# Performance work log

Hardware: AMD Instinct MI355X
Metric: run time of the kernel (lower is better)

Reference implementation:

```python
import jax, jax.numpy as jnp
import numpy as np
from jax import lax

RATES = (2, 3, 5, 9)
C_IN = 64
B, H, W = 4, 128, 128


def conv2d(x, w, b, dilation):
    # x: [B,C,H,W], w: [O,I,3,3]; padding=dilation keeps spatial size
    y = lax.conv_general_dilated(
        x, w, window_strides=(1, 1),
        padding=[(dilation, dilation), (dilation, dilation)],
        rhs_dilation=(dilation, dilation),
        dimension_numbers=('NCHW', 'OIHW', 'NCHW'))
    return y + b[None, :, None, None]


def bilinear_sample(x, py, px):
    # x: [B,C,H,W]; py,px: [B,K,H,W] float sampling positions; zeros outside
    Hh, Ww = x.shape[-2], x.shape[-1]
    y0 = jnp.floor(py)
    x0 = jnp.floor(px)
    wy1 = py - y0
    wx1 = px - x0
    wy0 = 1.0 - wy1
    wx0 = 1.0 - wx1

    def gather(yi, xi):
        valid = (yi >= 0) & (yi < Hh) & (xi >= 0) & (xi < Ww)
        yc = jnp.clip(yi, 0, Hh - 1).astype(jnp.int32)
        xc = jnp.clip(xi, 0, Ww - 1).astype(jnp.int32)
        # per-batch fancy gather: [C,K,H,W]
        vals = jax.vmap(lambda im, yy, xx: im[:, yy, xx])(x, yc, xc)
        return vals * valid[:, None].astype(x.dtype)

    out = (gather(y0, x0) * (wy0 * wx0)[:, None]
           + gather(y0, x0 + 1) * (wy0 * wx1)[:, None]
           + gather(y0 + 1, x0) * (wy1 * wx0)[:, None]
           + gather(y0 + 1, x0 + 1) * (wy1 * wx1)[:, None])
    return out  # [B,C,K,H,W]


def deform_conv(x, offset, weight, dilation):
    # offset: [B,18,H,W] = (dy,dx) per kernel point; weight: [O,C,3,3]
    b, c, h, w = x.shape
    K = 9
    off = offset.reshape(b, K, 2, h, w)
    dy, dx = off[:, :, 0], off[:, :, 1]
    ky = jnp.repeat((jnp.arange(3) - 1) * dilation, 3).astype(x.dtype)  # [9]
    kx = jnp.tile((jnp.arange(3) - 1) * dilation, 3).astype(x.dtype)
    hh = jnp.arange(h, dtype=x.dtype)[None, None, :, None]
    ww = jnp.arange(w, dtype=x.dtype)[None, None, None, :]
    py = hh + ky[None, :, None, None] + dy
    px = ww + kx[None, :, None, None] + dx
    sampled = bilinear_sample(x, py, px)  # [B,C,K,H,W]
    w9 = weight.reshape(weight.shape[0], c, K)
    return jnp.einsum('bckhw,ock->bohw', sampled, w9)


def setup_inputs() -> dict:
    key = jax.random.key(0)
    ks = jax.random.split(key, 8)
    s = 0.05
    return {
        'x': jax.random.normal(ks[0], (B, C_IN, H, W), jnp.float32),
        'dw': jax.random.normal(ks[1], (4, C_IN, C_IN, 3, 3), jnp.float32) * s,
        'ow': jax.random.normal(ks[2], (4, 18, C_IN, 3, 3), jnp.float32) * s,
        'ob': jax.random.normal(ks[3], (4, 18), jnp.float32) * s,
        'se_w1': jax.random.normal(ks[4], (C_IN, 4 * C_IN), jnp.float32) * s,
        'se_b1': jax.random.normal(ks[5], (C_IN,), jnp.float32) * s,
        'se_w2': jax.random.normal(ks[6], (4 * C_IN, C_IN), jnp.float32) * s,
        'se_b2': jax.random.normal(ks[7], (4 * C_IN,), jnp.float32) * s,
    }


def reference(x, dw, ow, ob, se_w1, se_b1, se_w2, se_b2):
    b, c, h, w = x.shape
    outs = []
    for i in range(4):
        j = (i - 1) % 4  # faithful to `self.offsets[i - 1]` in the source
        off = jax.nn.relu(conv2d(x, ow[j], ob[j], RATES[j]))
        outs.append(deform_conv(x, off, dw[i], RATES[i]))
    cat = jnp.concatenate(outs, axis=1)  # [B,4C,H,W]
    # SENet on concatenated features
    g = cat.mean(axis=(2, 3))  # [B,4C]
    h1 = jax.nn.relu(g @ se_w1.T + se_b1)
    s = jax.nn.sigmoid(h1 @ se_w2.T + se_b2)  # [B,4C]
    gated = (1.0 + s)[:, :, None, None] * cat
    fused = gated.reshape(b, 4, c, h, w).sum(axis=1)  # sum over the 4 stages
    return x + fused
```

## Files before the change

kernel.cpp:

```cpp
#include <hip/hip_runtime.h>
#include <hip/hip_bf16.h>
#include <math.h>

#define BATCH 4
#define CIN 64
#define HH 128
#define WW 128
#define HWP (HH*WW)

#define OFF_OFF   0
#define CAT_OFF   4718592
#define XHWC_OFF  (CAT_OFF + 8388608)
#define WTH_OFF   (XHWC_OFF + 2097152)
#define OWH_OFF   (WTH_OFF + 73728)
#define G_OFF     (OWH_OFF + 36864)
#define SCALE_OFF (G_OFF + 1024)

typedef _Float16 h16x2 __attribute__((ext_vector_type(2)));
typedef _Float16 h16x8 __attribute__((ext_vector_type(8)));
typedef float    f32x4 __attribute__((ext_vector_type(4)));

union h8view { h16x8 v8; h16x2 v2[4]; };

__device__ __forceinline__ int rate_of(int i) {
    return (i == 0) ? 2 : (i == 1) ? 3 : (i == 2) ? 5 : 9;
}

__global__ __launch_bounds__(256) void prep_kernel(
    const float* __restrict__ dw, const float* __restrict__ ow,
    _Float16* __restrict__ wth, _Float16* __restrict__ owh)
{
    int idx = blockIdx.x * 256 + threadIdx.x;
    if (idx < 147456) {
        int c = idx & 63;
        int k = (idx >> 6) % 9;
        int r = idx / 576;
        int o = r & 63;
        int i = r >> 6;
        wth[idx] = (_Float16)dw[((i * 64 + o) * 64 + c) * 9 + k];
        return;
    }
    int idx2 = idx - 147456;
    if (idx2 < 73728) {
        int c = idx2 & 63;
        int r = idx2 >> 6;
        int o = r & 31;
        int r2 = r >> 5;
        int tap = r2 % 9;
        int j = r2 / 9;
        owh[idx2] = (o < 18) ? (_Float16)ow[((j * 18 + o) * 64 + c) * 9 + tap]
                             : (_Float16)0.f;
    }
}

__global__ __launch_bounds__(256) void xhwc_kernel(
    const float* __restrict__ x, _Float16* __restrict__ xhwc)
{
    const int t  = threadIdx.x;
    const int b  = blockIdx.y;
    const int p0 = blockIdx.x * 64;
    const int px = t & 63;
    const int cO = t >> 6;

    const float* xb = x + (size_t)b * CIN * HWP + p0 + px;
    _Float16* xh = xhwc + ((size_t)b * HWP + p0 + px) * 64;

#pragma unroll
    for (int g = 0; g < 2; ++g) {
        const int cb = cO * 8 + g * 32;
        h16x8 v;
#pragma unroll
        for (int cj = 0; cj < 8; ++cj)
            v[cj] = (_Float16)xb[(size_t)(cb + cj) * HWP];
        *(h16x8*)(xh + cb) = v;
    }
}

__global__ __launch_bounds__(256) void offset_mfma_kernel(
    const _Float16* __restrict__ xhwc, const _Float16* __restrict__ owh,
    const float* __restrict__ ob, float* __restrict__ off)
{
    __shared__ __align__(16) _Float16 S2[2][64][72];

    const int t  = threadIdx.x;
    const int z  = blockIdx.y;
    const int j  = z >> 2, b = z & 3;
    const int d  = rate_of(j);
    const int p0 = blockIdx.x * 64;
    const int ph = p0 >> 7;
    const int cb0 = p0 & 127;

    const int wv = t >> 6, lane = t & 63;
    const int nl = lane & 15, quad = lane >> 4;

    const _Float16* xh = xhwc + (size_t)b * HWP * 64;

    f32x4 acc[2];
    acc[0] = (f32x4){0.f, 0.f, 0.f, 0.f};
    acc[1] = (f32x4){0.f, 0.f, 0.f, 0.f};

    h16x8 v[2];

    auto stage_load = [&](int kk) {
        const int iy = kk / 3, ix = kk % 3;
        const int ys = ph + (iy - 1) * d;
        const bool rowok = (unsigned)ys < (unsigned)HH;
#pragma unroll
        for (int q = 0; q < 2; ++q) {
            const int task = q * 256 + t;
            const int px = task >> 3, ch = task & 7;
            const int xs = cb0 + px + (ix - 1) * d;
            h16x8 vv = {};
            if (rowok && (unsigned)xs < (unsigned)WW)
                vv = *(const h16x8*)(xh + ((size_t)(ys * WW + xs)) * 64 + ch * 8);
            v[q] = vv;
        }
    };
    auto stage_store = [&](int buf) {
#pragma unroll
        for (int q = 0; q < 2; ++q) {
            const int task = q * 256 + t;
            const int px = task >> 3, ch = task & 7;
            *(h16x8*)&S2[buf][px][ch * 8] = v[q];
        }
    };

    stage_load(0);
    stage_store(0);
    __syncthreads();

    for (int k = 0; k < 9; ++k) {
        if (k < 8) stage_load(k + 1);

#pragma unroll
        for (int q2 = 0; q2 < 2; ++q2) {
            h16x8 a = *(const h16x8*)&S2[k & 1][wv * 16 + nl][q2 * 32 + quad * 8];
#pragma unroll
            for (int nt = 0; nt < 2; ++nt) {
                const _Float16* brow = owh
                    + ((size_t)((j * 9 + k) * 32 + nt * 16 + nl)) * 64;
                h16x8 bf = *(const h16x8*)&brow[q2 * 32 + quad * 8];
                acc[nt] = __builtin_amdgcn_mfma_f32_16x16x32_f16(a, bf, acc[nt], 0, 0, 0);
            }
        }

        if (k < 8) stage_store((k + 1) & 1);
        __syncthreads();
    }

    float* op = off + (size_t)z * 18 * HWP + p0;
#pragma unroll
    for (int nt = 0; nt < 2; ++nt) {
        const int o = nt * 16 + nl;
        if (o < 18) {
            const float bias = ob[j * 18 + o];
#pragma unroll
            for (int r = 0; r < 4; ++r) {
                const int pxl = wv * 16 + quad * 4 + r;
                op[(size_t)o * HWP + pxl] = fmaxf(acc[nt][r] + bias, 0.f);
            }
        }
    }
}

__global__ __launch_bounds__(256) void deform_mfma_kernel(
    const _Float16* __restrict__ xhwc, const _Float16* __restrict__ wth,
    const float* __restrict__ off, _Float16* __restrict__ cat)
{
    __shared__ __align__(16) _Float16 S[2][128][72];

    const int t  = threadIdx.x;
    const int z  = blockIdx.y;
    const int i  = z >> 2, b = z & 3;
    const int d  = rate_of(i);
    const int j  = (i + 3) & 3;
    const int ty = blockIdx.x >> 1;
    const int tx = blockIdx.x & 1;

    const int chunk = t & 7;
    const int pxb   = t >> 3;
    const int cb    = chunk * 8;

    const int wv = t >> 6, lane = t & 63;
    const int nl = lane & 15, quad = lane >> 4;

    const _Float16* xh = xhwc + (size_t)b * HWP * 64;
    const float* offb = off + ((size_t)(j * 4 + b) * 18) * HWP;

    int phv[4], pwv[4], pgv[4];
#pragma unroll
    for (int it = 0; it < 4; ++it) {
        const int psub = it * 32 + pxb;
        phv[it] = ty * 2 + (psub >> 6);
        pwv[it] = tx * 64 + (psub & 63);
        pgv[it] = phv[it] * WW + pwv[it];
    }

    f32x4 acc[8];
#pragma unroll
    for (int a = 0; a < 8; ++a) acc[a] = (f32x4){0.f, 0.f, 0.f, 0.f};

    h8view u[4][4];
    h16x2  wp[4][4];
    float  ocy[4], ocx[4];
    float  ony[4], onx[4];

    auto gather = [&](int kk) {
        const int iy = kk / 3, ix = kk % 3;
#pragma unroll
        for (int it = 0; it < 4; ++it) {
            float py = (float)(phv[it] + (iy - 1) * d) + ocy[it];
            float px = (float)(pwv[it] + (ix - 1) * d) + ocx[it];
            float fy0 = floorf(py), fx0 = floorf(px);
            float wy1 = py - fy0, wx1 = px - fx0;
            float wy0 = 1.f - wy1, wx0 = 1.f - wx1;
            int y0 = (int)fy0, x0 = (int)fx0;
            int y1 = y0 + 1,  x1 = x0 + 1;
            bool vy0 = (unsigned)y0 < (unsigned)HH, vy1 = (unsigned)y1 < (unsigned)HH;
            bool vx0 = (unsigned)x0 < (unsigned)WW, vx1 = (unsigned)x1 < (unsigned)WW;
            int yc0 = min(max(y0, 0), HH - 1), yc1 = min(max(y1, 0), HH - 1);
            int xc0 = min(max(x0, 0), WW - 1), xc1 = min(max(x1, 0), WW - 1);
            float w00 = (vy0 && vx0) ? wy0 * wx0 : 0.f;
            float w01 = (vy0 && vx1) ? wy0 * wx1 : 0.f;
            float w10 = (vy1 && vx0) ? wy1 * wx0 : 0.f;
            float w11 = (vy1 && vx1) ? wy1 * wx1 : 0.f;
            const _Float16 h00 = (_Float16)w00, h01 = (_Float16)w01;
            const _Float16 h10 = (_Float16)w10, h11 = (_Float16)w11;
            wp[it][0] = (h16x2){h00, h00};
            wp[it][1] = (h16x2){h01, h01};
            wp[it][2] = (h16x2){h10, h10};
            wp[it][3] = (h16x2){h11, h11};
            u[it][0].v8 = *(const h16x8*)(xh + (size_t)(yc0 * WW + xc0) * 64 + cb);
            u[it][1].v8 = *(const h16x8*)(xh + (size_t)(yc0 * WW + xc1) * 64 + cb);
            u[it][2].v8 = *(const h16x8*)(xh + (size_t)(yc1 * WW + xc0) * 64 + cb);
            u[it][3].v8 = *(const h16x8*)(xh + (size_t)(yc1 * WW + xc1) * 64 + cb);
        }
    };

    auto blendstore = [&](int buf) {
#pragma unroll
        for (int it = 0; it < 4; ++it) {
            h8view outv;
#pragma unroll
            for (int pp = 0; pp < 4; ++pp)
                outv.v2[pp] = u[it][0].v2[pp] * wp[it][0] + u[it][1].v2[pp] * wp[it][1]
                            + u[it][2].v2[pp] * wp[it][2] + u[it][3].v2[pp] * wp[it][3];
            *(h16x8*)&S[buf][it * 32 + pxb][cb] = outv.v8;
        }
    };

#pragma unroll
    for (int it = 0; it < 4; ++it) {
        ocy[it] = offb[0 * HWP + pgv[it]];
        ocx[it] = offb[1 * HWP + pgv[it]];
    }
    gather(0);
    blendstore(0);
#pragma unroll
    for (int it = 0; it < 4; ++it) {
        ocy[it] = offb[2 * HWP + pgv[it]];
        ocx[it] = offb[3 * HWP + pgv[it]];
    }
    __syncthreads();

    for (int k = 0; k < 9; ++k) {
        if (k < 8) {
            gather(k + 1);
            if (k < 7) {
#pragma unroll
                for (int it = 0; it < 4; ++it) {
                    ony[it] = offb[(2 * (k + 2)) * HWP + pgv[it]];
                    onx[it] = offb[(2 * (k + 2) + 1) * HWP + pgv[it]];
                }
            }
        }

#pragma unroll
        for (int q2 = 0; q2 < 2; ++q2) {
            h16x8 b0 = *(const h16x8*)&S[k & 1][wv * 32 + nl][q2 * 32 + quad * 8];
            h16x8 b1 = *(const h16x8*)&S[k & 1][wv * 32 + 16 + nl][q2 * 32 + quad * 8];
#pragma unroll
            for (int mt = 0; mt < 4; ++mt) {
                const _Float16* wrow = wth
                    + ((size_t)((i * 64 + mt * 16 + nl) * 9 + k)) * 64;
                h16x8 a = *(const h16x8*)&wrow[q2 * 32 + quad * 8];
                acc[mt * 2 + 0] = __builtin_amdgcn_mfma_f32_16x16x32_f16(a, b0, acc[mt * 2 + 0], 0, 0, 0);
                acc[mt * 2 + 1] = __builtin_amdgcn_mfma_f32_16x16x32_f16(a, b1, acc[mt * 2 + 1], 0, 0, 0);
            }
        }

        if (k < 8) {
            blendstore((k + 1) & 1);
#pragma unroll
            for (int it = 0; it < 4; ++it) { ocy[it] = ony[it]; ocx[it] = onx[it]; }
        }
        __syncthreads();
    }

#pragma unroll
    for (int mt = 0; mt < 4; ++mt) {
#pragma unroll
        for (int nt = 0; nt < 2; ++nt) {
            const int psub = wv * 32 + nt * 16 + nl;
            const int prow = ty * 2 + (psub >> 6);
            const int pcol = tx * 64 + (psub & 63);
            _Float16* cp = cat
                + ((size_t)(b * 256 + i * 64 + mt * 16 + quad * 4)) * HWP
                + prow * WW + pcol;
            const f32x4 v = acc[mt * 2 + nt];
#pragma unroll
            for (int r = 0; r < 4; ++r)
                cp[(size_t)r * HWP] = (_Float16)v[r];
        }
    }
}

__global__ __launch_bounds__(256) void reduce_kernel(
    const _Float16* __restrict__ cat, float* __restrict__ g)
{
    const int bc = blockIdx.x;
    const _Float16* p = cat + (size_t)bc * HWP;
    float s = 0.f;
#pragma unroll
    for (int q = 0; q < 8; ++q) {
        h16x8 v8 = *(const h16x8*)(p + q * 2048 + threadIdx.x * 8);
#pragma unroll
        for (int e = 0; e < 8; ++e) s += (float)v8[e];
    }
#pragma unroll
    for (int o = 32; o > 0; o >>= 1) s += __shfl_down(s, o, 64);
    __shared__ float ls[4];
    if ((threadIdx.x & 63) == 0) ls[threadIdx.x >> 6] = s;
    __syncthreads();
    if (threadIdx.x == 0) {
        g[bc] = (ls[0] + ls[1] + ls[2] + ls[3]) * (1.f / (float)HWP);
    }
}

__global__ __launch_bounds__(256) void se_kernel(
    const float* __restrict__ g,  const float* __restrict__ w1,
    const float* __restrict__ b1, const float* __restrict__ w2,
    const float* __restrict__ b2, float* __restrict__ scale)
{
    __shared__ float gs[1024];
    __shared__ float h1s[256];
    const int t = threadIdx.x;
#pragma unroll
    for (int q = 0; q < 4; ++q) gs[q * 256 + t] = g[q * 256 + t];
    __syncthreads();
    {
        int b = t >> 6, o = t & 63;
        float a = b1[o];
        for (int c = 0; c < 256; ++c)
            a = fmaf(gs[b * 256 + c], w1[o * 256 + c], a);
        h1s[t] = fmaxf(a, 0.f);
    }
    __syncthreads();
#pragma unroll
    for (int q = 0; q < 4; ++q) {
        int idx = q * 256 + t;
        int b = idx >> 8, cc = idx & 255;
        float a = b2[cc];
#pragma unroll 8
        for (int o = 0; o < 64; ++o)
            a = fmaf(h1s[b * 64 + o], w2[cc * 64 + o], a);
        scale[idx] = 1.f + 1.f / (1.f + expf(-a));
    }
}

__global__ __launch_bounds__(256) void final_kernel(
    const float* __restrict__ x, const _Float16* __restrict__ cat,
    const float* __restrict__ scale, float* __restrict__ out)
{
    const int gid = blockIdx.x;
    const int p = (gid & 63) * 256 + threadIdx.x;
    const int c = (gid >> 6) & 63;
    const int b = gid >> 12;
    const float s0 = scale[b * 256 + c];
    const float s1 = scale[b * 256 + 64 + c];
    const float s2 = scale[b * 256 + 128 + c];
    const float s3 = scale[b * 256 + 192 + c];
    const _Float16* cb = cat + ((size_t)(b * 256 + c)) * HWP + p;
    float v = x[(size_t)(b * 64 + c) * HWP + p];
    v = fmaf(s0, (float)cb[0 * 64 * HWP], v);
    v = fmaf(s1, (float)cb[1 * 64 * HWP], v);
    v = fmaf(s2, (float)cb[2 * 64 * HWP], v);
    v = fmaf(s3, (float)cb[3 * 64 * HWP], v);
    out[(size_t)(b * 64 + c) * HWP + p] = v;
}

extern "C" void kernel_launch(void* const* d_in, const int* in_sizes, int n_in,
                              void* d_out, int out_size, void* d_ws, size_t ws_size,
                              hipStream_t stream) {
    const float* x  = (const float*)d_in[0];
    const float* dw = (const float*)d_in[1];
    const float* ow = (const float*)d_in[2];
    const float* ob = (const float*)d_in[3];
    const float* w1 = (const float*)d_in[4];
    const float* b1 = (const float*)d_in[5];
    const float* w2 = (const float*)d_in[6];
    const float* b2 = (const float*)d_in[7];
    float* out = (float*)d_out;
    float* ws  = (float*)d_ws;

    float* OFF      = ws + OFF_OFF;
    _Float16* CAT   = (_Float16*)(ws + CAT_OFF);
    _Float16* XHWC  = (_Float16*)(ws + XHWC_OFF);
    _Float16* WTH   = (_Float16*)(ws + WTH_OFF);
    _Float16* OWH   = (_Float16*)(ws + OWH_OFF);
    float* G        = ws + G_OFF;
    float* SCALE    = ws + SCALE_OFF;

    prep_kernel<<<864, 256, 0, stream>>>(dw, ow, WTH, OWH);
    xhwc_kernel<<<dim3(256, 4), 256, 0, stream>>>(x, XHWC);
    offset_mfma_kernel<<<dim3(256, 16), 256, 0, stream>>>(XHWC, OWH, ob, OFF);
    deform_mfma_kernel<<<dim3(128, 16), 256, 0, stream>>>(XHWC, WTH, OFF, CAT);
    reduce_kernel<<<1024, 256, 0, stream>>>(CAT, G);
    se_kernel<<<1, 256, 0, stream>>>(G, w1, b1, w2, b2, SCALE);
    final_kernel<<<16384, 256, 0, stream>>>(x, CAT, SCALE, out);
}
```

Baseline: 305.4 us.

## Reuse staged halo row across kx taps in offset conv; single-buffer LDS

The offset convolution now stages one input row with a 2*d halo per kernel row (3 stages instead of 9), so the three horizontal taps read shifted windows from the same LDS tile instead of reloading from global memory. Both the offset and deform kernels drop from double-buffered to single-buffered shared memory and add an extra barrier before each store. This cuts global loads and LDS footprint, which may raise occupancy, at the cost of more synchronisation and less overlap between loads and MFMA work.

```diff
diff --git a/kernel.cpp b/kernel.cpp
--- a/kernel.cpp
+++ b/kernel.cpp
@@ -80,7 +80,7 @@
     const _Float16* __restrict__ xhwc, const _Float16* __restrict__ owh,
     const float* __restrict__ ob, float* __restrict__ off)
 {
-    __shared__ __align__(16) _Float16 S2[2][64][72];
+    __shared__ __align__(16) _Float16 S2[82][72];
 
     const int t  = threadIdx.x;
     const int z  = blockIdx.y;
@@ -95,56 +95,67 @@
 
     const _Float16* xh = xhwc + (size_t)b * HWP * 64;
 
+    const int width = 64 + 2 * d;
+    const int ntask = width * 8;
+
     f32x4 acc[2];
     acc[0] = (f32x4){0.f, 0.f, 0.f, 0.f};
     acc[1] = (f32x4){0.f, 0.f, 0.f, 0.f};
 
-    h16x8 v[2];
-
-    auto stage_load = [&](int kk) {
-        const int iy = kk / 3, ix = kk % 3;
-        const int ys = ph + (iy - 1) * d;
+    h16x8 sv[3];
+
+    auto stage_load = [&](int g) {
+        const int ys = ph + (g - 1) * d;
         const bool rowok = (unsigned)ys < (unsigned)HH;
 #pragma unroll
-        for (int q = 0; q < 2; ++q) {
+        for (int q = 0; q < 3; ++q) {
             const int task = q * 256 + t;
-            const int px = task >> 3, ch = task & 7;
-            const int xs = cb0 + px + (ix - 1) * d;
             h16x8 vv = {};
-            if (rowok && (unsigned)xs < (unsigned)WW)
-                vv = *(const h16x8*)(xh + ((size_t)(ys * WW + xs)) * 64 + ch * 8);
-            v[q] = vv;
+            if (task < ntask) {
+                const int sp = task >> 3, ch = task & 7;
+                const int xs = cb0 - d + sp;
+                if (rowok && (unsigned)xs < (unsigned)WW)
+                    vv = *(const h16x8*)(xh + ((size_t)(ys * WW + xs)) * 64 + ch * 8);
+            }
+            sv[q] = vv;
         }
     };
-    auto stage_store = [&](int buf) {
-#pragma unroll
-        for (int q = 0; q < 2; ++q) {
+    auto stage_store = [&]() {
+#pragma unroll
+        for (int q = 0; q < 3; ++q) {
             const int task = q * 256 + t;
-            const int px = task >> 3, ch = task & 7;
-            *(h16x8*)&S2[buf][px][ch * 8] = v[q];
+            if (task < ntask) {
+                const int sp = task >> 3, ch = task & 7;
+                *(h16x8*)&S2[sp][ch * 8] = sv[q];
+            }
         }
     };
 
     stage_load(0);
-    stage_store(0);
+    stage_store();
     __syncthreads();
 
-    for (int k = 0; k < 9; ++k) {
-        if (k < 8) stage_load(k + 1);
-
-#pragma unroll
-        for (int q2 = 0; q2 < 2; ++q2) {
-            h16x8 a = *(const h16x8*)&S2[k & 1][wv * 16 + nl][q2 * 32 + quad * 8];
-#pragma unroll
-            for (int nt = 0; nt < 2; ++nt) {
-                const _Float16* brow = owh
-                    + ((size_t)((j * 9 + k) * 32 + nt * 16 + nl)) * 64;
-                h16x8 bf = *(const h16x8*)&brow[q2 * 32 + quad * 8];
-                acc[nt] = __builtin_amdgcn_mfma_f32_16x16x32_f16(a, bf, acc[nt], 0, 0, 0);
-            }
-        }
-
-        if (k < 8) stage_store((k + 1) & 1);
+    for (int g = 0; g < 3; ++g) {
+        if (g < 2) stage_load(g + 1);
+
+#pragma unroll
+        for (int ix = 0; ix < 3; ++ix) {
+            const int k = g * 3 + ix;
+#pragma unroll
+            for (int q2 = 0; q2 < 2; ++q2) {
+                h16x8 a = *(const h16x8*)&S2[wv * 16 + nl + ix * d][q2 * 32 + quad * 8];
+#pragma unroll
+                for (int nt = 0; nt < 2; ++nt) {
+                    const _Float16* brow = owh
+                        + ((size_t)((j * 9 + k) * 32 + nt * 16 + nl)) * 64;
+                    h16x8 bf = *(const h16x8*)&brow[q2 * 32 + quad * 8];
+                    acc[nt] = __builtin_amdgcn_mfma_f32_16x16x32_f16(a, bf, acc[nt], 0, 0, 0);
+                }
+            }
+        }
+
+        __syncthreads();
+        if (g < 2) stage_store();
         __syncthreads();
     }
 
@@ -167,7 +178,7 @@
     const _Float16* __restrict__ xhwc, const _Float16* __restrict__ wth,
     const float* __restrict__ off, _Float16* __restrict__ cat)
 {
-    __shared__ __align__(16) _Float16 S[2][128][72];
+    __shared__ __align__(16) _Float16 S[128][72];
 
     const int t  = threadIdx.x;
     const int z  = blockIdx.y;
@@ -237,7 +248,7 @@
         }
     };
 
-    auto blendstore = [&](int buf) {
+    auto blendstore = [&]() {
 #pragma unroll
         for (int it = 0; it < 4; ++it) {
             h8view outv;
@@ -245,7 +256,7 @@
             for (int pp = 0; pp < 4; ++pp)
                 outv.v2[pp] = u[it][0].v2[pp] * wp[it][0] + u[it][1].v2[pp] * wp[it][1]
                             + u[it][2].v2[pp] * wp[it][2] + u[it][3].v2[pp] * wp[it][3];
-            *(h16x8*)&S[buf][it * 32 + pxb][cb] = outv.v8;
+            *(h16x8*)&S[it * 32 + pxb][cb] = outv.v8;
         }
     };
 
@@ -255,7 +266,7 @@
         ocx[it] = offb[1 * HWP + pgv[it]];
     }
     gather(0);
-    blendstore(0);
+    blendstore();
 #pragma unroll
     for (int it = 0; it < 4; ++it) {
         ocy[it] = offb[2 * HWP + pgv[it]];
@@ -277,8 +288,8 @@
 
 #pragma unroll
         for (int q2 = 0; q2 < 2; ++q2) {
-            h16x8 b0 = *(const h16x8*)&S[k & 1][wv * 32 + nl][q2 * 32 + quad * 8];
-            h16x8 b1 = *(const h16x8*)&S[k & 1][wv * 32 + 16 + nl][q2 * 32 + quad * 8];
+            h16x8 b0 = *(const h16x8*)&S[wv * 32 + nl][q2 * 32 + quad * 8];
+            h16x8 b1 = *(const h16x8*)&S[wv * 32 + 16 + nl][q2 * 32 + quad * 8];
 #pragma unroll
             for (int mt = 0; mt < 4; ++mt) {
                 const _Float16* wrow = wth
@@ -289,8 +300,9 @@
             }
         }
 
+        __syncthreads();
         if (k < 8) {
-            blendstore((k + 1) & 1);
+            blendstore();
 #pragma unroll
             for (int it = 0; it < 4; ++it) { ocy[it] = ony[it]; ocx[it] = onx[it]; }
         }
```

After: 305.8 us. About the same (+0.1%).
